# Kernel optimization log

Hardware: AMD Instinct MI355X
Metric: run time of the kernel (lower is better)

## Reference

```python
import jax, jax.numpy as jnp
import numpy as np

B = 4096
N_FEATS = 2048
N_TAGS = 300
RNN_IN = 512
RNN_HID = 512
HID = 512


def setup_inputs() -> dict:
    key = jax.random.key(0)
    ks = jax.random.split(key, 16)
    sc = 0.05  # small weight init, like get_init_weights
    inp = {
        "v": jax.random.normal(ks[0], (B, N_FEATS), jnp.float32),
        "s": jax.random.normal(ks[1], (B, N_TAGS), jnp.float32),
        "decoder_input": jax.random.normal(ks[2], (B, RNN_IN), jnp.float32),
        "rnn_h": jax.random.normal(ks[3], (B, HID), jnp.float32),
        "rnn_c": jax.random.normal(ks[4], (B, HID), jnp.float32),
        # gate axis g=4 stacks (i, f, o, c); per-gate math is independent,
        # identical to the original per-gate weight matrices.
        "Wa": jax.random.normal(ks[5], (4, RNN_IN, RNN_HID), jnp.float32) * sc,
        "Wb": jax.random.normal(ks[6], (4, N_TAGS, RNN_HID), jnp.float32) * sc,
        "Wc": jax.random.normal(ks[7], (4, RNN_HID, HID), jnp.float32) * sc,
        "Ua": jax.random.normal(ks[8], (4, HID, RNN_HID), jnp.float32) * sc,
        "Ub": jax.random.normal(ks[9], (4, N_TAGS, RNN_HID), jnp.float32) * sc,
        "Uc": jax.random.normal(ks[10], (4, RNN_HID, HID), jnp.float32) * sc,
        "Ca": jax.random.normal(ks[11], (4, N_FEATS, RNN_HID), jnp.float32) * sc,
        "Cb": jax.random.normal(ks[12], (4, N_TAGS, RNN_HID), jnp.float32) * sc,
        "Cc": jax.random.normal(ks[13], (4, RNN_HID, HID), jnp.float32) * sc,
        "b": jnp.zeros((4, HID), jnp.float32),
    }
    return inp


def _step(v, s, x, h, c, Wa, Wb, Wc, Ua, Ub, Uc, Ca, Cb, Cc, b):
    # precompute_mats: tag/visual branch projections (gate-stacked)
    t2 = jnp.einsum("bt,gtr->gbr", s, Wb)   # s @ Wb_*
    t3 = jnp.einsum("bf,gfr->gbr", v, Ca)   # v @ Ca_*
    t4 = jnp.einsum("bt,gtr->gbr", s, Cb)   # s @ Cb_*
    # forward: input/hidden branch projections
    t1 = jnp.einsum("bi,gir->gbr", x, Wa)   # x @ Wa_*
    t5 = jnp.einsum("bt,gtr->gbr", s, Ub)   # s @ Ub_*
    t6 = jnp.einsum("bh,ghr->gbr", h, Ua)   # h @ Ua_*
    # bilinear fusion then second-stage projection per gate
    logits = (
        jnp.einsum("gbr,grh->gbh", t1 * t2, Wc)
        + jnp.einsum("gbr,grh->gbh", t3 * t4, Cc)
        + jnp.einsum("gbr,grh->gbh", t5 * t6, Uc)
        + b[:, None, :]
    )
    i = jax.nn.sigmoid(logits[0])
    f = jax.nn.sigmoid(logits[1])
    o = jax.nn.sigmoid(logits[2])
    g = jnp.tanh(logits[3])
    new_c = f * c + i * g
    new_h = o * jnp.tanh(new_c)
    return new_h, new_c


def reference(v, s, decoder_input, rnn_h, rnn_c, Wa, Wb, Wc, Ua, Ub, Uc, Ca, Cb, Cc, b):
    return _step(v, s, decoder_input, rnn_h, rnn_c, Wa, Wb, Wc, Ua, Ub, Uc, Ca, Cb, Cc, b)
```

## Files before the change

kernel.cpp:

```cpp
#include <hip/hip_runtime.h>
#include <hip/hip_bf16.h>
#include <stdint.h>

#define B_DIM 4096
#define NFEATS 2048
#define NTAGS 300
#define NTAGSP 320
#define RIN 512
#define RHID 512
#define HIDD 512
#define KCAT 1536
#define NGATE_N 2048

typedef __attribute__((ext_vector_type(8))) short short8;
typedef __attribute__((ext_vector_type(8))) unsigned short ushort8;
typedef __attribute__((ext_vector_type(4))) float f32x4;

typedef __attribute__((address_space(3))) unsigned int lds_u32_t;
typedef __attribute__((address_space(1))) const unsigned int glb_u32_t;

__device__ __forceinline__ unsigned short f2bf(float f) {
  union { float f; unsigned u; } x; x.f = f;
  unsigned r = (x.u + 0x7fffu + ((x.u >> 16) & 1u)) >> 16;
  return (unsigned short)r;
}

__device__ __forceinline__ void gl2lds16(const void* g, void* l) {
  __builtin_amdgcn_global_load_lds((glb_u32_t*)g, (lds_u32_t*)l, 16, 0, 0);
}

__global__ void cvt_all(const float* __restrict__ v, const float* __restrict__ x,
                        const float* __restrict__ h, const float* __restrict__ s,
                        unsigned short* __restrict__ vb, unsigned short* __restrict__ xb,
                        unsigned short* __restrict__ hb, unsigned short* __restrict__ sb) {
  int seg = blockIdx.y;
  const float* src; unsigned short* dst; int sc, dc;
  if (seg == 0)      { src = v; dst = vb; sc = NFEATS; dc = NFEATS; }
  else if (seg == 1) { src = x; dst = xb; sc = RIN;    dc = RIN; }
  else if (seg == 2) { src = h; dst = hb; sc = RHID;   dc = RHID; }
  else               { src = s; dst = sb; sc = NTAGS;  dc = NTAGSP; }
  int cpr = dc >> 3;
  long nch = (long)B_DIM * cpr;
  for (long i = (long)blockIdx.x * blockDim.x + threadIdx.x; i < nch;
       i += (long)gridDim.x * blockDim.x) {
    int r = (int)(i / cpr);
    int c0 = (int)(i - (long)r * cpr) << 3;
    const float* sp = src + (long)r * sc + c0;
    ushort8 o;
#pragma unroll
    for (int j = 0; j < 8; ++j) {
      float f = (c0 + j < sc) ? sp[j] : 0.f;
      o[j] = f2bf(f);
    }
    *(ushort8*)(dst + (i << 3)) = o;
  }
}

struct TD { const float* src; unsigned short* dst; int K; int dstLd; int dstOff; int kx0; };
struct TP { TD d[9]; };

__global__ void trans_all(TP tp) {
  __shared__ float t[32][33];
  int bx = blockIdx.x;
  int m = 0;
#pragma unroll
  for (int i = 1; i < 9; ++i)
    if (bx >= tp.d[i].kx0) m = i;
  TD td = tp.d[m];
  int g = blockIdx.z;
  const float* s = td.src + (long)g * td.K * 512;
  unsigned short* d = td.dst + (long)g * 512 * td.dstLd;
  int k0 = (bx - td.kx0) * 32, n0 = blockIdx.y * 32;
  int tx = threadIdx.x, ty = threadIdx.y;
#pragma unroll
  for (int r = 0; r < 4; ++r) {
    int k = k0 + ty + r * 8;
    t[ty + r * 8][tx] = (k < td.K) ? s[(long)k * 512 + n0 + tx] : 0.f;
  }
  __syncthreads();
#pragma unroll
  for (int r = 0; r < 4; ++r) {
    int n = n0 + ty + r * 8;
    d[(long)n * td.dstLd + td.dstOff + k0 + tx] = f2bf(t[tx][ty + r * 8]);
  }
}

#define BM 128
#define BN 128
#define BK 32

__device__ __forceinline__ void stage_tile(const unsigned short* __restrict__ g, int ld,
                                           int rowBase, int k0, unsigned short* lds, int tid) {
#pragma unroll
  for (int j = 0; j < 2; ++j) {
    int chunk = j * 256 + tid;
    int row = chunk >> 2;
    int kc = (chunk & 3) << 3;
    const unsigned short* src = g + (long)(rowBase + row) * ld + (k0 + kc);
    unsigned short* dst = lds + ((j * 256 + (tid & ~63)) << 3);
    gl2lds16(src, dst);
  }
}

__device__ __forceinline__ void mma_tile(const unsigned short* As, const unsigned short* Bs,
                                         f32x4 acc[4][4], int wr, int wc, int lr, int lg) {
  short8 a[4], b[4];
#pragma unroll
  for (int mi = 0; mi < 4; ++mi)
    a[mi] = *(const short8*)(As + (wr + mi * 16 + lr) * BK + lg * 8);
#pragma unroll
  for (int ni = 0; ni < 4; ++ni)
    b[ni] = *(const short8*)(Bs + (wc + ni * 16 + lr) * BK + lg * 8);
#pragma unroll
  for (int mi = 0; mi < 4; ++mi)
#pragma unroll
    for (int ni = 0; ni < 4; ++ni)
      acc[mi][ni] = __builtin_amdgcn_mfma_f32_16x16x32_bf16(a[mi], b[ni], acc[mi][ni], 0, 0, 0);
}

__device__ __forceinline__ void gemm_loop(const unsigned short* __restrict__ A,
                                          const unsigned short* __restrict__ Bt, int K,
                                          int rowBase, int colBase,
                                          unsigned short* As, unsigned short* Bs,
                                          f32x4 acc[4][4], int tid, int wr, int wc, int lr, int lg) {
  for (int k0 = 0; k0 < K; k0 += BK) {
    __syncthreads();
    stage_tile(A, K, rowBase, k0, As, tid);
    stage_tile(Bt, K, colBase, k0, Bs, tid);
    __syncthreads();
    mma_tile(As, Bs, acc, wr, wc, lr, lg);
  }
}

__global__ __launch_bounds__(256) void gemm_s1_all(
    const unsigned short* __restrict__ vb, const unsigned short* __restrict__ xb,
    const unsigned short* __restrict__ hb, const unsigned short* __restrict__ sb,
    const unsigned short* __restrict__ CaT, const unsigned short* __restrict__ WaT,
    const unsigned short* __restrict__ UaT,
    const unsigned short* __restrict__ CbT, const unsigned short* __restrict__ WbT,
    const unsigned short* __restrict__ UbT,
    unsigned short* __restrict__ P) {
  __shared__ __align__(16) unsigned short As[BM * BK];
  __shared__ __align__(16) unsigned short Bs[BN * BK];
  int z = blockIdx.z;
  const unsigned short *A1, *B1t, *B2t;
  int K1, coff;
  if (z == 0)      { A1 = vb; B1t = CaT; K1 = NFEATS; B2t = CbT; coff = 512; }
  else if (z == 1) { A1 = xb; B1t = WaT; K1 = RIN;    B2t = WbT; coff = 0; }
  else             { A1 = hb; B1t = UaT; K1 = RHID;   B2t = UbT; coff = 1024; }

  int tid = threadIdx.x;
  int l = tid & 63, w = tid >> 6;
  int wr = (w >> 1) * 64, wc = (w & 1) * 64, lr = l & 15, lg = l >> 4;
  int rowBase = blockIdx.x * BM, colBase = blockIdx.y * BN;

  f32x4 acc1[4][4], acc2[4][4];
#pragma unroll
  for (int mi = 0; mi < 4; ++mi)
#pragma unroll
    for (int ni = 0; ni < 4; ++ni)
#pragma unroll
      for (int r = 0; r < 4; ++r) { acc1[mi][ni][r] = 0.f; acc2[mi][ni][r] = 0.f; }

  gemm_loop(A1, B1t, K1, rowBase, colBase, As, Bs, acc1, tid, wr, wc, lr, lg);
  gemm_loop(sb, B2t, NTAGSP, rowBase, colBase, As, Bs, acc2, tid, wr, wc, lr, lg);

  int gate = colBase >> 9;
  unsigned short* Pg = P + (long)gate * B_DIM * KCAT;
#pragma unroll
  for (int mi = 0; mi < 4; ++mi)
#pragma unroll
    for (int ni = 0; ni < 4; ++ni) {
      int colg = colBase + wc + ni * 16 + lr;
      int col = coff + (colg & 511);
#pragma unroll
      for (int r = 0; r < 4; ++r) {
        int row = rowBase + wr + mi * 16 + lg * 4 + r;
        float pv = acc1[mi][ni][r] * acc2[mi][ni][r];
        Pg[(long)row * KCAT + col] = f2bf(pv);
      }
    }
}

__global__ __launch_bounds__(256) void gemm_s2(
    const unsigned short* __restrict__ P, const unsigned short* __restrict__ WcT,
    const float* __restrict__ bias, float* __restrict__ logits) {
  __shared__ __align__(16) unsigned short As[BM * BK];
  __shared__ __align__(16) unsigned short Bs[BN * BK];
  int tid = threadIdx.x;
  int l = tid & 63, w = tid >> 6;
  int wr = (w >> 1) * 64, wc = (w & 1) * 64, lr = l & 15, lg = l >> 4;
  int g = blockIdx.z;
  int rowBase = blockIdx.x * BM, colBase = blockIdx.y * BN;

  f32x4 acc[4][4];
#pragma unroll
  for (int mi = 0; mi < 4; ++mi)
#pragma unroll
    for (int ni = 0; ni < 4; ++ni)
#pragma unroll
      for (int r = 0; r < 4; ++r) acc[mi][ni][r] = 0.f;

  gemm_loop(P + (long)g * B_DIM * KCAT, WcT + (long)g * 512 * KCAT, KCAT,
            rowBase, colBase, As, Bs, acc, tid, wr, wc, lr, lg);

  const float* bg = bias + g * HIDD;
  float* Lg = logits + (long)g * B_DIM * HIDD;
#pragma unroll
  for (int mi = 0; mi < 4; ++mi)
#pragma unroll
    for (int ni = 0; ni < 4; ++ni) {
      int col = colBase + wc + ni * 16 + lr;
      float bv = bg[col];
#pragma unroll
      for (int r = 0; r < 4; ++r) {
        int row = rowBase + wr + mi * 16 + lg * 4 + r;
        Lg[(long)row * HIDD + col] = acc[mi][ni][r] + bv;
      }
    }
}

__global__ void lstm_final(const float* __restrict__ logits, const float* __restrict__ c_in,
                           float* __restrict__ out) {
  const long GS = (long)B_DIM * HIDD;
  long i = (long)blockIdx.x * blockDim.x + threadIdx.x;
  if (i >= (GS >> 2)) return;
  f32x4 l0 = *(const f32x4*)(logits + 4 * i);
  f32x4 l1 = *(const f32x4*)(logits + GS + 4 * i);
  f32x4 l2 = *(const f32x4*)(logits + 2 * GS + 4 * i);
  f32x4 l3 = *(const f32x4*)(logits + 3 * GS + 4 * i);
  f32x4 cv = *(const f32x4*)(c_in + 4 * i);
  f32x4 ho, co;
#pragma unroll
  for (int r = 0; r < 4; ++r) {
    float ig = 1.f / (1.f + __expf(-l0[r]));
    float fg = 1.f / (1.f + __expf(-l1[r]));
    float og = 1.f / (1.f + __expf(-l2[r]));
    float gg = tanhf(l3[r]);
    float c = fg * cv[r] + ig * gg;
    co[r] = c;
    ho[r] = og * tanhf(c);
  }
  *(f32x4*)(out + 4 * i) = ho;
  *(f32x4*)(out + GS + 4 * i) = co;
}

extern "C" void kernel_launch(void* const* d_in, const int* in_sizes, int n_in,
                              void* d_out, int out_size, void* d_ws, size_t ws_size,
                              hipStream_t stream) {
  const float* v  = (const float*)d_in[0];
  const float* s  = (const float*)d_in[1];
  const float* x  = (const float*)d_in[2];
  const float* h  = (const float*)d_in[3];
  const float* c  = (const float*)d_in[4];
  const float* Wa = (const float*)d_in[5];
  const float* Wb = (const float*)d_in[6];
  const float* Wc = (const float*)d_in[7];
  const float* Ua = (const float*)d_in[8];
  const float* Ub = (const float*)d_in[9];
  const float* Uc = (const float*)d_in[10];
  const float* Ca = (const float*)d_in[11];
  const float* Cb = (const float*)d_in[12];
  const float* Cc = (const float*)d_in[13];
  const float* bb = (const float*)d_in[14];
  float* out = (float*)d_out;

  char* ws = (char*)d_ws;
  size_t off = 0;
  auto alloc = [&](size_t bytes) {
    char* p = ws + off;
    off = (off + bytes + 255) & ~(size_t)255;
    return p;
  };
  unsigned short* vb    = (unsigned short*)alloc((size_t)B_DIM * NFEATS * 2);
  unsigned short* sb    = (unsigned short*)alloc((size_t)B_DIM * NTAGSP * 2);
  unsigned short* xb    = (unsigned short*)alloc((size_t)B_DIM * RIN * 2);
  unsigned short* hb    = (unsigned short*)alloc((size_t)B_DIM * RHID * 2);
  unsigned short* WaT   = (unsigned short*)alloc((size_t)4 * 512 * 512 * 2);
  unsigned short* WbT   = (unsigned short*)alloc((size_t)4 * 512 * NTAGSP * 2);
  unsigned short* UaT   = (unsigned short*)alloc((size_t)4 * 512 * 512 * 2);
  unsigned short* UbT   = (unsigned short*)alloc((size_t)4 * 512 * NTAGSP * 2);
  unsigned short* CaT   = (unsigned short*)alloc((size_t)4 * 512 * NFEATS * 2);
  unsigned short* CbT   = (unsigned short*)alloc((size_t)4 * 512 * NTAGSP * 2);
  unsigned short* WcatT = (unsigned short*)alloc((size_t)4 * 512 * KCAT * 2);
  unsigned short* Pbuf  = (unsigned short*)alloc((size_t)4 * B_DIM * KCAT * 2);
  float*          Lg    = (float*)alloc((size_t)4 * B_DIM * HIDD * 4);

  cvt_all<<<dim3(512, 4), 256, 0, stream>>>(v, x, h, s, vb, xb, hb, sb);

  TP tp;
  tp.d[0] = { Wa, WaT,   512, 512,  0,    0   };
  tp.d[1] = { Wb, WbT,   300, 320,  0,    16  };
  tp.d[2] = { Ua, UaT,   512, 512,  0,    26  };
  tp.d[3] = { Ub, UbT,   300, 320,  0,    42  };
  tp.d[4] = { Ca, CaT,  2048, 2048, 0,    52  };
  tp.d[5] = { Cb, CbT,   300, 320,  0,    116 };
  tp.d[6] = { Wc, WcatT, 512, 1536, 0,    126 };
  tp.d[7] = { Cc, WcatT, 512, 1536, 512,  142 };
  tp.d[8] = { Uc, WcatT, 512, 1536, 1024, 158 };
  trans_all<<<dim3(174, 16, 4), dim3(32, 8), 0, stream>>>(tp);

  gemm_s1_all<<<dim3(B_DIM / BM, NGATE_N / BN, 3), 256, 0, stream>>>(
      vb, xb, hb, sb, CaT, WaT, UaT, CbT, WbT, UbT, Pbuf);

  gemm_s2<<<dim3(B_DIM / BM, HIDD / BN, 4), 256, 0, stream>>>(Pbuf, WcatT, bb, Lg);

  lstm_final<<<(B_DIM * HIDD / 4 + 255) / 256, 256, 0, stream>>>(Lg, c, out);
}
```

Before: 200.7 us.

## Split tag projections into own GEMM and use 256x256 pipelined MFMA tiles

Replaces the 128x128 single-buffered GEMMs with a 256x256, 512-thread core that uses 128KB of LDS, double-buffers with a swizzled layout, and interleaves async global-to-LDS loads with MFMA quarters. The s-branch projections (Wb, Cb, Ub) are computed once by a separate GEMM into a bf16 buffer. The bilinear GEMM then multiplies by that buffer in its epilogue, so it no longer runs two K-loops per tile. This targets low MFMA utilisation and sync stalls from the small tiles. In exchange it adds an extra bf16 round-trip of the tag products through global memory, and the large grids may leave CUs underused (384 blocks at 2 per CU).

```diff
diff --git a/kernel.cpp b/kernel.cpp
--- a/kernel.cpp
+++ b/kernel.cpp
@@ -10,7 +10,6 @@
 #define RHID 512
 #define HIDD 512
 #define KCAT 1536
-#define NGATE_N 2048
 
 typedef __attribute__((ext_vector_type(8))) short short8;
 typedef __attribute__((ext_vector_type(8))) unsigned short ushort8;
@@ -24,10 +23,23 @@
   unsigned r = (x.u + 0x7fffu + ((x.u >> 16) & 1u)) >> 16;
   return (unsigned short)r;
 }
+__device__ __forceinline__ float bf2f(unsigned short u) {
+  union { unsigned u; float f; } x; x.u = ((unsigned)u) << 16;
+  return x.f;
+}
 
 __device__ __forceinline__ void gl2lds16(const void* g, void* l) {
   __builtin_amdgcn_global_load_lds((glb_u32_t*)g, (lds_u32_t*)l, 16, 0, 0);
 }
+
+__device__ __forceinline__ void sbar() {
+  asm volatile("" ::: "memory");
+  __builtin_amdgcn_s_barrier();
+  asm volatile("" ::: "memory");
+}
+#define VMCNT4()   asm volatile("s_waitcnt vmcnt(4)" ::: "memory")
+#define VMCNT0()   asm volatile("s_waitcnt vmcnt(0)" ::: "memory")
+#define LGKMCNT0() asm volatile("s_waitcnt lgkmcnt(0)" ::: "memory")
 
 __global__ void cvt_all(const float* __restrict__ v, const float* __restrict__ x,
                         const float* __restrict__ h, const float* __restrict__ s,
@@ -85,138 +97,207 @@
   }
 }
 
-#define BM 128
-#define BN 128
-#define BK 32
-
-__device__ __forceinline__ void stage_tile(const unsigned short* __restrict__ g, int ld,
-                                           int rowBase, int k0, unsigned short* lds, int tid) {
-#pragma unroll
-  for (int j = 0; j < 2; ++j) {
-    int chunk = j * 256 + tid;
-    int row = chunk >> 2;
-    int kc = (chunk & 3) << 3;
-    const unsigned short* src = g + (long)(rowBase + row) * ld + (k0 + kc);
-    unsigned short* dst = lds + ((j * 256 + (tid & ~63)) << 3);
-    gl2lds16(src, dst);
-  }
-}
-
-__device__ __forceinline__ void mma_tile(const unsigned short* As, const unsigned short* Bs,
-                                         f32x4 acc[4][4], int wr, int wc, int lr, int lg) {
-  short8 a[4], b[4];
-#pragma unroll
-  for (int mi = 0; mi < 4; ++mi)
-    a[mi] = *(const short8*)(As + (wr + mi * 16 + lr) * BK + lg * 8);
-#pragma unroll
-  for (int ni = 0; ni < 4; ++ni)
-    b[ni] = *(const short8*)(Bs + (wc + ni * 16 + lr) * BK + lg * 8);
-#pragma unroll
-  for (int mi = 0; mi < 4; ++mi)
+
+__device__ __forceinline__ void stage_half(const unsigned short* mat, int ld,
+                                           int gRow0, int k0, char* ldsHalf,
+                                           int rl0, int scb, int dstoff) {
+  const char* s0 = (const char*)(mat + (long)(gRow0 + rl0) * ld + k0) + scb;
+  const char* s1 = (const char*)(mat + (long)(gRow0 + 64 + rl0) * ld + k0) + scb;
+  gl2lds16(s0, ldsHalf + dstoff);
+  gl2lds16(s1, ldsHalf + 8192 + dstoff);
+}
+
+__device__ __forceinline__ void mfma_q(f32x4 (&acc)[8][4], int mb, int nb,
+                                       const short8 (&af)[4][2], const short8 (&bf)[2][2]) {
+  __builtin_amdgcn_s_setprio(1);
+#pragma unroll
+  for (int m = 0; m < 4; ++m)
+#pragma unroll
+    for (int n = 0; n < 2; ++n)
+#pragma unroll
+      for (int kk = 0; kk < 2; ++kk)
+        acc[mb + m][nb + n] =
+            __builtin_amdgcn_mfma_f32_16x16x32_bf16(af[m][kk], bf[n][kk], acc[mb + m][nb + n], 0, 0, 0);
+  __builtin_amdgcn_s_setprio(0);
+}
+
+__device__ __forceinline__ void gemm8_core(const unsigned short* __restrict__ A, int lda,
+                                           const unsigned short* __restrict__ Bm, int ldb,
+                                           int nt, int rowBase, int colBase,
+                                           char* smem, int tid, f32x4 (&acc)[8][4]) {
+  char* Ab0 = smem;
+  char* Bb0 = smem + 65536;
+  int l = tid & 63, w = tid >> 6;
+  int wr = w >> 2, wc = w & 3;
+  int lr = l & 15, lg = l >> 4;
+  int LA = lr * 128 + ((lg * 16) ^ ((lr & 7) << 4));
+  int rl0 = tid >> 3;
+  int scb = ((tid & 7) << 4) ^ ((rl0 & 7) << 4);
+  int dstoff = (tid & ~63) << 4;
+
+#pragma unroll
+  for (int mi = 0; mi < 8; ++mi)
 #pragma unroll
     for (int ni = 0; ni < 4; ++ni)
-      acc[mi][ni] = __builtin_amdgcn_mfma_f32_16x16x32_bf16(a[mi], b[ni], acc[mi][ni], 0, 0, 0);
-}
-
-__device__ __forceinline__ void gemm_loop(const unsigned short* __restrict__ A,
-                                          const unsigned short* __restrict__ Bt, int K,
-                                          int rowBase, int colBase,
-                                          unsigned short* As, unsigned short* Bs,
-                                          f32x4 acc[4][4], int tid, int wr, int wc, int lr, int lg) {
-  for (int k0 = 0; k0 < K; k0 += BK) {
-    __syncthreads();
-    stage_tile(A, K, rowBase, k0, As, tid);
-    stage_tile(Bt, K, colBase, k0, Bs, tid);
-    __syncthreads();
-    mma_tile(As, Bs, acc, wr, wc, lr, lg);
-  }
-}
-
-__global__ __launch_bounds__(256) void gemm_s1_all(
+#pragma unroll
+      for (int r = 0; r < 4; ++r) acc[mi][ni][r] = 0.f;
+
+  stage_half(A, lda, rowBase, 0, Ab0, rl0, scb, dstoff);
+  stage_half(A, lda, rowBase + 128, 0, Ab0 + 16384, rl0, scb, dstoff);
+  stage_half(Bm, ldb, colBase, 0, Bb0, rl0, scb, dstoff);
+  stage_half(Bm, ldb, colBase + 128, 0, Bb0 + 16384, rl0, scb, dstoff);
+  if (nt > 1) {
+    stage_half(A, lda, rowBase, 64, Ab0 + 32768, rl0, scb, dstoff);
+    stage_half(A, lda, rowBase + 128, 64, Ab0 + 49152, rl0, scb, dstoff);
+    VMCNT4();
+  } else {
+    VMCNT0();
+  }
+  sbar();
+
+  for (int g = 0; g < nt; ++g) {
+    int cur = g & 1;
+    char* Ab = Ab0 + cur * 32768 + wr * 16384;
+    char* Bb = Bb0 + cur * 32768 + wc * 8192;
+    char* BbN = Bb0 + (cur ^ 1) * 32768;
+    short8 a[4][2], b0[2][2], b1[2][2];
+
+#pragma unroll
+    for (int m = 0; m < 4; ++m) {
+      a[m][0] = *(const short8*)(Ab + m * 2048 + LA);
+      a[m][1] = *(const short8*)(Ab + m * 2048 + (LA ^ 64));
+    }
+#pragma unroll
+    for (int n = 0; n < 2; ++n) {
+      b0[n][0] = *(const short8*)(Bb + n * 2048 + LA);
+      b0[n][1] = *(const short8*)(Bb + n * 2048 + (LA ^ 64));
+    }
+    if (g + 1 < nt) stage_half(Bm, ldb, colBase, (g + 1) * 64, BbN, rl0, scb, dstoff);
+    sbar();
+    LGKMCNT0();
+    mfma_q(acc, 0, 0, a, b0);
+    sbar();
+
+#pragma unroll
+    for (int n = 0; n < 2; ++n) {
+      b1[n][0] = *(const short8*)(Bb + 4096 + n * 2048 + LA);
+      b1[n][1] = *(const short8*)(Bb + 4096 + n * 2048 + (LA ^ 64));
+    }
+    if (g + 1 < nt) stage_half(Bm, ldb, colBase + 128, (g + 1) * 64, BbN + 16384, rl0, scb, dstoff);
+    sbar();
+    LGKMCNT0();
+    mfma_q(acc, 0, 2, a, b1);
+    sbar();
+
+#pragma unroll
+    for (int m = 0; m < 4; ++m) {
+      a[m][0] = *(const short8*)(Ab + 8192 + m * 2048 + LA);
+      a[m][1] = *(const short8*)(Ab + 8192 + m * 2048 + (LA ^ 64));
+    }
+    sbar();
+    LGKMCNT0();
+    mfma_q(acc, 4, 2, a, b1);
+    sbar();
+
+    if (g + 2 < nt) {
+      stage_half(A, lda, rowBase, (g + 2) * 64, Ab0 + cur * 32768, rl0, scb, dstoff);
+      stage_half(A, lda, rowBase + 128, (g + 2) * 64, Ab0 + cur * 32768 + 16384, rl0, scb, dstoff);
+    }
+    mfma_q(acc, 4, 0, a, b0);
+    if (g + 2 < nt) { VMCNT4(); } else if (g + 1 < nt) { VMCNT0(); }
+    sbar();
+  }
+}
+
+
+__global__ __launch_bounds__(512, 2) void gemm_ts(const unsigned short* __restrict__ sb,
+                                                  const unsigned short* __restrict__ SBT,
+                                                  unsigned short* __restrict__ TS) {
+  extern __shared__ char smem[];
+  int tid = threadIdx.x;
+  int rowBase = blockIdx.x * 256, colBase = blockIdx.y * 256;
+  f32x4 acc[8][4];
+  gemm8_core(sb, NTAGSP, SBT, NTAGSP, 5, rowBase, colBase, smem, tid, acc);
+
+  int l = tid & 63, w = tid >> 6, wr = w >> 2, wc = w & 3, lr = l & 15, lg = l >> 4;
+  int branch = colBase >> 11;
+  unsigned short* TSb = TS + (long)branch * B_DIM * 2048;
+#pragma unroll
+  for (int mi = 0; mi < 8; ++mi)
+#pragma unroll
+    for (int ni = 0; ni < 4; ++ni) {
+      int colg = (colBase & 2047) + wc * 64 + ni * 16 + lr;
+      int row0 = rowBase + wr * 128 + mi * 16 + lg * 4;
+#pragma unroll
+      for (int r = 0; r < 4; ++r)
+        TSb[(long)(row0 + r) * 2048 + colg] = f2bf(acc[mi][ni][r]);
+    }
+}
+
+__global__ __launch_bounds__(512, 2) void gemm_bil(
     const unsigned short* __restrict__ vb, const unsigned short* __restrict__ xb,
-    const unsigned short* __restrict__ hb, const unsigned short* __restrict__ sb,
+    const unsigned short* __restrict__ hb,
     const unsigned short* __restrict__ CaT, const unsigned short* __restrict__ WaT,
     const unsigned short* __restrict__ UaT,
-    const unsigned short* __restrict__ CbT, const unsigned short* __restrict__ WbT,
-    const unsigned short* __restrict__ UbT,
-    unsigned short* __restrict__ P) {
-  __shared__ __align__(16) unsigned short As[BM * BK];
-  __shared__ __align__(16) unsigned short Bs[BN * BK];
-  int z = blockIdx.z;
-  const unsigned short *A1, *B1t, *B2t;
-  int K1, coff;
-  if (z == 0)      { A1 = vb; B1t = CaT; K1 = NFEATS; B2t = CbT; coff = 512; }
-  else if (z == 1) { A1 = xb; B1t = WaT; K1 = RIN;    B2t = WbT; coff = 0; }
-  else             { A1 = hb; B1t = UaT; K1 = RHID;   B2t = UbT; coff = 1024; }
-
+    const unsigned short* __restrict__ TS, unsigned short* __restrict__ P) {
+  extern __shared__ char smem[];
   int tid = threadIdx.x;
-  int l = tid & 63, w = tid >> 6;
-  int wr = (w >> 1) * 64, wc = (w & 1) * 64, lr = l & 15, lg = l >> 4;
-  int rowBase = blockIdx.x * BM, colBase = blockIdx.y * BN;
-
-  f32x4 acc1[4][4], acc2[4][4];
-#pragma unroll
-  for (int mi = 0; mi < 4; ++mi)
-#pragma unroll
-    for (int ni = 0; ni < 4; ++ni)
-#pragma unroll
-      for (int r = 0; r < 4; ++r) { acc1[mi][ni][r] = 0.f; acc2[mi][ni][r] = 0.f; }
-
-  gemm_loop(A1, B1t, K1, rowBase, colBase, As, Bs, acc1, tid, wr, wc, lr, lg);
-  gemm_loop(sb, B2t, NTAGSP, rowBase, colBase, As, Bs, acc2, tid, wr, wc, lr, lg);
-
-  int gate = colBase >> 9;
-  unsigned short* Pg = P + (long)gate * B_DIM * KCAT;
-#pragma unroll
-  for (int mi = 0; mi < 4; ++mi)
+  int z = blockIdx.y >> 3;
+  int rowBase = blockIdx.x * 256, colBase = (blockIdx.y & 7) * 256;
+  const unsigned short *A1, *B1;
+  int K1, nt, coff;
+  if (z == 0)      { A1 = vb; B1 = CaT; K1 = NFEATS; nt = 32; coff = 512; }
+  else if (z == 1) { A1 = xb; B1 = WaT; K1 = RIN;    nt = 8;  coff = 0; }
+  else             { A1 = hb; B1 = UaT; K1 = RHID;   nt = 8;  coff = 1024; }
+
+  f32x4 acc[8][4];
+  gemm8_core(A1, K1, B1, K1, nt, rowBase, colBase, smem, tid, acc);
+
+  int l = tid & 63, w = tid >> 6, wr = w >> 2, wc = w & 3, lr = l & 15, lg = l >> 4;
+  const unsigned short* TSz = TS + (long)z * B_DIM * 2048;
+#pragma unroll
+  for (int mi = 0; mi < 8; ++mi)
 #pragma unroll
     for (int ni = 0; ni < 4; ++ni) {
-      int colg = colBase + wc + ni * 16 + lr;
+      int colg = colBase + wc * 64 + ni * 16 + lr;
+      int gate = colg >> 9;
       int col = coff + (colg & 511);
+      int row0 = rowBase + wr * 128 + mi * 16 + lg * 4;
+      unsigned short* Pg = P + (long)gate * B_DIM * KCAT;
 #pragma unroll
       for (int r = 0; r < 4; ++r) {
-        int row = rowBase + wr + mi * 16 + lg * 4 + r;
-        float pv = acc1[mi][ni][r] * acc2[mi][ni][r];
-        Pg[(long)row * KCAT + col] = f2bf(pv);
+        float ts = bf2f(TSz[(long)(row0 + r) * 2048 + colg]);
+        Pg[(long)(row0 + r) * KCAT + col] = f2bf(acc[mi][ni][r] * ts);
       }
     }
 }
 
-__global__ __launch_bounds__(256) void gemm_s2(
-    const unsigned short* __restrict__ P, const unsigned short* __restrict__ WcT,
-    const float* __restrict__ bias, float* __restrict__ logits) {
-  __shared__ __align__(16) unsigned short As[BM * BK];
-  __shared__ __align__(16) unsigned short Bs[BN * BK];
+__global__ __launch_bounds__(512, 2) void gemm_lg(const unsigned short* __restrict__ P,
+                                                  const unsigned short* __restrict__ WcT,
+                                                  const float* __restrict__ bias,
+                                                  float* __restrict__ logits) {
+  extern __shared__ char smem[];
   int tid = threadIdx.x;
-  int l = tid & 63, w = tid >> 6;
-  int wr = (w >> 1) * 64, wc = (w & 1) * 64, lr = l & 15, lg = l >> 4;
-  int g = blockIdx.z;
-  int rowBase = blockIdx.x * BM, colBase = blockIdx.y * BN;
-
-  f32x4 acc[4][4];
-#pragma unroll
-  for (int mi = 0; mi < 4; ++mi)
-#pragma unroll
-    for (int ni = 0; ni < 4; ++ni)
-#pragma unroll
-      for (int r = 0; r < 4; ++r) acc[mi][ni][r] = 0.f;
-
-  gemm_loop(P + (long)g * B_DIM * KCAT, WcT + (long)g * 512 * KCAT, KCAT,
-            rowBase, colBase, As, Bs, acc, tid, wr, wc, lr, lg);
-
-  const float* bg = bias + g * HIDD;
-  float* Lg = logits + (long)g * B_DIM * HIDD;
-#pragma unroll
-  for (int mi = 0; mi < 4; ++mi)
+  int gate = blockIdx.z;
+  int rowBase = blockIdx.x * 256, colBase = blockIdx.y * 256;
+  const unsigned short* Pg  = P + (long)gate * B_DIM * KCAT;
+  const unsigned short* Wg  = WcT + (long)gate * 512 * KCAT;
+  f32x4 acc[8][4];
+  gemm8_core(Pg, KCAT, Wg, KCAT, 24, rowBase, colBase, smem, tid, acc);
+
+  int l = tid & 63, w = tid >> 6, wr = w >> 2, wc = w & 3, lr = l & 15, lg = l >> 4;
+  float* Lg = logits + (long)gate * B_DIM * HIDD;
+  const float* bg = bias + gate * HIDD;
+#pragma unroll
+  for (int mi = 0; mi < 8; ++mi)
 #pragma unroll
     for (int ni = 0; ni < 4; ++ni) {
-      int col = colBase + wc + ni * 16 + lr;
+      int col = colBase + wc * 64 + ni * 16 + lr;
       float bv = bg[col];
-#pragma unroll
-      for (int r = 0; r < 4; ++r) {
-        int row = rowBase + wr + mi * 16 + lg * 4 + r;
-        Lg[(long)row * HIDD + col] = acc[mi][ni][r] + bv;
-      }
+      int row0 = rowBase + wr * 128 + mi * 16 + lg * 4;
+#pragma unroll
+      for (int r = 0; r < 4; ++r)
+        Lg[(long)(row0 + r) * HIDD + col] = acc[mi][ni][r] + bv;
     }
 }
 
@@ -277,33 +358,35 @@
   unsigned short* xb    = (unsigned short*)alloc((size_t)B_DIM * RIN * 2);
   unsigned short* hb    = (unsigned short*)alloc((size_t)B_DIM * RHID * 2);
   unsigned short* WaT   = (unsigned short*)alloc((size_t)4 * 512 * 512 * 2);
-  unsigned short* WbT   = (unsigned short*)alloc((size_t)4 * 512 * NTAGSP * 2);
   unsigned short* UaT   = (unsigned short*)alloc((size_t)4 * 512 * 512 * 2);
-  unsigned short* UbT   = (unsigned short*)alloc((size_t)4 * 512 * NTAGSP * 2);
   unsigned short* CaT   = (unsigned short*)alloc((size_t)4 * 512 * NFEATS * 2);
-  unsigned short* CbT   = (unsigned short*)alloc((size_t)4 * 512 * NTAGSP * 2);
   unsigned short* WcatT = (unsigned short*)alloc((size_t)4 * 512 * KCAT * 2);
+  unsigned short* SBT   = (unsigned short*)alloc((size_t)3 * 2048 * NTAGSP * 2);
+  unsigned short* TSb   = (unsigned short*)alloc((size_t)3 * B_DIM * 2048 * 2);
   unsigned short* Pbuf  = (unsigned short*)alloc((size_t)4 * B_DIM * KCAT * 2);
-  float*          Lg    = (float*)alloc((size_t)4 * B_DIM * HIDD * 4);
+  float*          Lg    = (float*)TSb;
 
   cvt_all<<<dim3(512, 4), 256, 0, stream>>>(v, x, h, s, vb, xb, hb, sb);
 
   TP tp;
-  tp.d[0] = { Wa, WaT,   512, 512,  0,    0   };
-  tp.d[1] = { Wb, WbT,   300, 320,  0,    16  };
-  tp.d[2] = { Ua, UaT,   512, 512,  0,    26  };
-  tp.d[3] = { Ub, UbT,   300, 320,  0,    42  };
-  tp.d[4] = { Ca, CaT,  2048, 2048, 0,    52  };
-  tp.d[5] = { Cb, CbT,   300, 320,  0,    116 };
-  tp.d[6] = { Wc, WcatT, 512, 1536, 0,    126 };
-  tp.d[7] = { Cc, WcatT, 512, 1536, 512,  142 };
-  tp.d[8] = { Uc, WcatT, 512, 1536, 1024, 158 };
+  tp.d[0] = { Wa, WaT,                  512, 512,  0,    0   };
+  tp.d[1] = { Wb, SBT + 2048 * 320,     300, 320,  0,    16  };
+  tp.d[2] = { Ua, UaT,                  512, 512,  0,    26  };
+  tp.d[3] = { Ub, SBT + 2 * 2048 * 320, 300, 320,  0,    42  };
+  tp.d[4] = { Ca, CaT,                 2048, 2048, 0,    52  };
+  tp.d[5] = { Cb, SBT,                  300, 320,  0,    116 };
+  tp.d[6] = { Wc, WcatT,                512, 1536, 0,    126 };
+  tp.d[7] = { Cc, WcatT,                512, 1536, 512,  142 };
+  tp.d[8] = { Uc, WcatT,                512, 1536, 1024, 158 };
   trans_all<<<dim3(174, 16, 4), dim3(32, 8), 0, stream>>>(tp);
 
-  gemm_s1_all<<<dim3(B_DIM / BM, NGATE_N / BN, 3), 256, 0, stream>>>(
-      vb, xb, hb, sb, CaT, WaT, UaT, CbT, WbT, UbT, Pbuf);
-
-  gemm_s2<<<dim3(B_DIM / BM, HIDD / BN, 4), 256, 0, stream>>>(Pbuf, WcatT, bb, Lg);
+  hipFuncSetAttribute((const void*)gemm_ts,  hipFuncAttributeMaxDynamicSharedMemorySize, 131072);
+  hipFuncSetAttribute((const void*)gemm_bil, hipFuncAttributeMaxDynamicSharedMemorySize, 131072);
+  hipFuncSetAttribute((const void*)gemm_lg,  hipFuncAttributeMaxDynamicSharedMemorySize, 131072);
+
+  gemm_ts<<<dim3(16, 24), 512, 131072, stream>>>(sb, SBT, TSb);
+  gemm_bil<<<dim3(16, 24), 512, 131072, stream>>>(vb, xb, hb, CaT, WaT, UaT, TSb, Pbuf);
+  gemm_lg<<<dim3(16, 2, 4), 512, 131072, stream>>>(Pbuf, WcatT, bb, Lg);
 
   lstm_final<<<(B_DIM * HIDD / 4 + 255) / 256, 256, 0, stream>>>(Lg, c, out);
 }
```

New measurement: 197.9 us. Within noise of the previous version (-1.4%).
